# Optimization experiments

Measured on AMD Instinct MI355X. Metric: run time of the kernel, lower is better.

The kernel has to match this reference:

```python
import jax, jax.numpy as jnp
import numpy as np

N_NODES = 100000
N_EDGES = 3200000
IN_DIM = 768
HIDDEN = 128
CLASS_NUM = 2
N_GRAPHS = 512


def setup_inputs() -> dict:
    key = jax.random.key(0)
    ks = jax.random.split(key, 10)
    x = jax.random.normal(ks[0], (N_NODES, IN_DIM), dtype=jnp.float32)
    edge_index = jax.random.randint(ks[1], (2, N_EDGES), 0, N_NODES, dtype=jnp.int64)
    ptr = jnp.sort(jax.random.randint(ks[2], (N_GRAPHS + 1,), 0, N_NODES, dtype=jnp.int64))
    def glorot(k, shape):
        lim = jnp.sqrt(6.0 / (shape[0] + shape[1]))
        return jax.random.uniform(k, shape, jnp.float32, -lim, lim)
    W1 = glorot(ks[3], (IN_DIM, HIDDEN))
    b1 = jnp.zeros((HIDDEN,), jnp.float32)
    W2 = glorot(ks[4], (HIDDEN, HIDDEN))
    b2 = jnp.zeros((HIDDEN,), jnp.float32)
    Wc = glorot(ks[5], (HIDDEN, CLASS_NUM))
    bc = jnp.zeros((CLASS_NUM,), jnp.float32)
    return {"x": x, "edge_index": edge_index, "ptr": ptr,
            "W1": W1, "b1": b1, "W2": W2, "b2": b2, "Wc": Wc, "bc": bc}


def _gcn_conv(x, W, b, src, dst, norm, n_nodes):
    # PyG GCNConv: linear first, then normalized scatter-add aggregation, then bias
    h = x @ W                                  # [N, out]
    msg = h[src] * norm[:, None]               # gather + scale, [E+N, out]
    out = jax.ops.segment_sum(msg, dst, num_segments=n_nodes)
    return out + b


def reference(x, edge_index, ptr, W1, b1, W2, b2, Wc, bc):
    n = x.shape[0]
    loop = jnp.arange(n, dtype=edge_index.dtype)
    src = jnp.concatenate([edge_index[0], loop])  # add self-loops
    dst = jnp.concatenate([edge_index[1], loop])
    deg = jax.ops.segment_sum(jnp.ones_like(dst, dtype=x.dtype), dst, num_segments=n)
    dinv = jnp.where(deg > 0, jax.lax.rsqrt(deg), 0.0)
    norm = dinv[src] * dinv[dst]               # symmetric normalization
    h = jax.nn.relu(_gcn_conv(x, W1, b1, src, dst, norm, n))
    h = jax.nn.relu(_gcn_conv(h, W2, b2, src, dst, norm, n))
    out = _gcn_conv(h, Wc, bc, src, dst, norm, n)
    return out[ptr[:-1]]                       # first_pool: first node of each graph
```

## Files before the change

### kernel.cpp

```cpp
#include <hip/hip_runtime.h>

typedef short bf16x8 __attribute__((ext_vector_type(8)));
typedef float f32x4 __attribute__((ext_vector_type(4)));
typedef _Float16 f16x4 __attribute__((ext_vector_type(4)));

__device__ __forceinline__ unsigned short f2bf_rn(float x) {
    unsigned int u = __float_as_uint(x);
    unsigned int r = u + 0x7FFF + ((u >> 16) & 1);
    return (unsigned short)(r >> 16);
}
__device__ __forceinline__ float bf2f(unsigned short h) {
    return __uint_as_float(((unsigned int)h) << 16);
}


__global__ __launch_bounds__(256) void bucket_hist(const int* __restrict__ ei,
                                                   int* __restrict__ bcnt, int E, int NB) {
    __shared__ int h[1024];
    for (int i = threadIdx.x; i < NB; i += 256) h[i] = 0;
    __syncthreads();
    for (int e = blockIdx.x * blockDim.x + threadIdx.x; e < E; e += gridDim.x * blockDim.x) {
        atomicAdd(&h[ei[E + e] >> 7], 1);
    }
    __syncthreads();
    for (int i = threadIdx.x; i < NB; i += 256) {
        int v = h[i];
        if (v) atomicAdd(&bcnt[i], v);
    }
}

__global__ __launch_bounds__(1024) void bucket_scan(const int* __restrict__ bcnt,
                                                    int* __restrict__ bbase,
                                                    int* __restrict__ bcur,
                                                    int* __restrict__ offs,
                                                    int NB, int NN, int E) {
    __shared__ int s[1024];
    int t = threadIdx.x;
    int v = (t < NB) ? bcnt[t] : 0;
    s[t] = v;
    __syncthreads();
    for (int off = 1; off < 1024; off <<= 1) {
        int u = (t >= off) ? s[t - off] : 0;
        __syncthreads();
        s[t] += u;
        __syncthreads();
    }
    if (t < NB) {
        int base = s[t] - v;
        bbase[t] = base;
        bcur[t] = base;
    }
    if (t == 0) {
        bbase[NB] = E;
        offs[NN] = E;
    }
}

__global__ __launch_bounds__(256) void bucket_scatter(const int* __restrict__ ei,
                                                      int* __restrict__ bcur,
                                                      unsigned int* __restrict__ epk,
                                                      int E, int NB) {
    __shared__ int hist[1024];
    __shared__ int cur[1024];
    int tid = threadIdx.x;
    int chunk = (E + gridDim.x - 1) / gridDim.x;
    int beg = blockIdx.x * chunk;
    int end = beg + chunk; if (end > E) end = E;
    for (int i = tid; i < NB; i += 256) hist[i] = 0;
    __syncthreads();
    for (int e = beg + tid; e < end; e += 256) {
        atomicAdd(&hist[ei[E + e] >> 7], 1);
    }
    __syncthreads();
    for (int i = tid; i < NB; i += 256) {
        int c = hist[i];
        cur[i] = c ? atomicAdd(&bcur[i], c) : 0;
    }
    __syncthreads();
    for (int e = beg + tid; e < end; e += 256) {
        int s = ei[e];
        int d = ei[E + e];
        int p = atomicAdd(&cur[d >> 7], 1);
        epk[p] = ((unsigned)(d & 127) << 17) | (unsigned)s;
    }
}

__global__ __launch_bounds__(256) void bucket_build(const unsigned int* __restrict__ epk,
                                                    const int* __restrict__ bbase,
                                                    int* __restrict__ offs,
                                                    float* __restrict__ dinv,
                                                    int* __restrict__ srt,
                                                    int NN) {
    __shared__ int lcnt[128];
    __shared__ int sc[128];
    __shared__ int lcur[128];
    int b = blockIdx.x;
    int tid = threadIdx.x;
    int base = bbase[b], endp = bbase[b + 1];
    int ne = endp - base;
    int v0 = b << 7;
    int nv = NN - v0; if (nv > 128) nv = 128;

    if (tid < 128) lcnt[tid] = 0;
    __syncthreads();
    for (int i = tid; i < ne; i += 256) {
        int d = (int)(epk[base + i] >> 17);
        atomicAdd(&lcnt[d], 1);
    }
    __syncthreads();
    if (tid < 128) sc[tid] = lcnt[tid];
    __syncthreads();
    for (int off = 1; off < 128; off <<= 1) {
        int u = (tid < 128 && tid >= off) ? sc[tid - off] : 0;
        __syncthreads();
        if (tid < 128) sc[tid] += u;
        __syncthreads();
    }
    if (tid < nv) {
        int ex = sc[tid] - lcnt[tid];
        offs[v0 + tid] = base + ex;
        lcur[tid] = base + ex;
        dinv[v0 + tid] = rsqrtf((float)(lcnt[tid] + 1));
    }
    __syncthreads();
    for (int i = tid; i < ne; i += 256) {
        unsigned int pk = epk[base + i];
        int d = (int)(pk >> 17);
        int s = (int)(pk & 0x1FFFFu);
        int p = atomicAdd(&lcur[d], 1);
        srt[p] = s;
    }
}

__global__ void wt_prep(const float* __restrict__ W, unsigned short* __restrict__ hi,
                        unsigned short* __restrict__ lo, int K) {
    int idx = blockIdx.x * 256 + threadIdx.x;
    if (idx >= K * 128) return;
    int k = idx >> 7;
    int c = idx & 127;
    float x = W[idx];
    unsigned short h = f2bf_rn(x);
    unsigned short l = f2bf_rn(x - bf2f(h));
    hi[(size_t)c * K + k] = h;
    lo[(size_t)c * K + k] = l;
}

template <int K>
__global__ __launch_bounds__(256) void gemm_mfma(const float* __restrict__ X,
                                                 const unsigned short* __restrict__ Wt_hi,
                                                 const unsigned short* __restrict__ Wt_lo,
                                                 const float* __restrict__ dinv,
                                                 _Float16* __restrict__ G, int n) {
    __shared__ unsigned short As_hi[128][40];
    __shared__ unsigned short As_lo[128][40];
    __shared__ unsigned short Bs_hi[128][40];
    __shared__ unsigned short Bs_lo[128][40];

    const int tid = threadIdx.x;
    const int wave = tid >> 6;
    const int lane = tid & 63;
    const int l15 = lane & 15;
    const int l4 = lane >> 4;
    const int row0 = blockIdx.x * 128;
    const int wr0 = wave * 32;
    const size_t plane = (size_t)n * 16;

    f32x4 acc[2][8];
#pragma unroll
    for (int i = 0; i < 2; ++i)
#pragma unroll
        for (int j = 0; j < 8; ++j) acc[i][j] = (f32x4){0.f, 0.f, 0.f, 0.f};

    const int sr = tid >> 1;
    const int sf = (tid & 1) * 16;

    for (int k0 = 0; k0 < K; k0 += 32) {
        __syncthreads();
        {
            int grow = row0 + sr;
            float4 v[4];
            if (grow < n) {
                const float* src = X + (size_t)grow * K + k0 + sf;
#pragma unroll
                for (int g = 0; g < 4; ++g) v[g] = *(const float4*)(src + g * 4);
            } else {
#pragma unroll
                for (int g = 0; g < 4; ++g) v[g] = make_float4(0.f, 0.f, 0.f, 0.f);
            }
#pragma unroll
            for (int g = 0; g < 4; ++g) {
                ushort4 h, l;
                h.x = f2bf_rn(v[g].x); l.x = f2bf_rn(v[g].x - bf2f(h.x));
                h.y = f2bf_rn(v[g].y); l.y = f2bf_rn(v[g].y - bf2f(h.y));
                h.z = f2bf_rn(v[g].z); l.z = f2bf_rn(v[g].z - bf2f(h.z));
                h.w = f2bf_rn(v[g].w); l.w = f2bf_rn(v[g].w - bf2f(h.w));
                *(ushort4*)&As_hi[sr][sf + g * 4] = h;
                *(ushort4*)&As_lo[sr][sf + g * 4] = l;
            }
        }
        {
#pragma unroll
            for (int rep = 0; rep < 2; ++rep) {
                int id = tid + rep * 256;
                int c = id >> 2;
                int q = (id & 3) * 8;
                *(uint4*)&Bs_hi[c][q] = *(const uint4*)&Wt_hi[(size_t)c * K + k0 + q];
                *(uint4*)&Bs_lo[c][q] = *(const uint4*)&Wt_lo[(size_t)c * K + k0 + q];
            }
        }
        __syncthreads();
        bf16x8 ah[2], al[2];
#pragma unroll
        for (int i = 0; i < 2; ++i) {
            ah[i] = *(const bf16x8*)&As_hi[wr0 + i * 16 + l15][l4 * 8];
            al[i] = *(const bf16x8*)&As_lo[wr0 + i * 16 + l15][l4 * 8];
        }
#pragma unroll
        for (int j = 0; j < 8; ++j) {
            bf16x8 bh = *(const bf16x8*)&Bs_hi[j * 16 + l15][l4 * 8];
            bf16x8 bl = *(const bf16x8*)&Bs_lo[j * 16 + l15][l4 * 8];
#pragma unroll
            for (int i = 0; i < 2; ++i) {
                acc[i][j] = __builtin_amdgcn_mfma_f32_16x16x32_bf16(ah[i], bh, acc[i][j], 0, 0, 0);
                acc[i][j] = __builtin_amdgcn_mfma_f32_16x16x32_bf16(ah[i], bl, acc[i][j], 0, 0, 0);
                acc[i][j] = __builtin_amdgcn_mfma_f32_16x16x32_bf16(al[i], bh, acc[i][j], 0, 0, 0);
            }
        }
    }
#pragma unroll
    for (int i = 0; i < 2; ++i) {
#pragma unroll
        for (int r = 0; r < 4; ++r) {
            int grow = row0 + wr0 + i * 16 + l4 * 4 + r;
            if (grow < n) {
                float dv = dinv[grow];
#pragma unroll
                for (int j = 0; j < 8; ++j) {
                    G[plane * j + (size_t)grow * 16 + l15] = (_Float16)(acc[i][j][r] * dv);
                }
            }
        }
    }
}

__global__ __launch_bounds__(256) void aggregate_slice4(const _Float16* __restrict__ G,
                                                        const int* __restrict__ offs,
                                                        const int* __restrict__ srt,
                                                        const float* __restrict__ dinv,
                                                        const float* __restrict__ bias,
                                                        float* __restrict__ H, int n, int do_relu) {
    int bid = blockIdx.x;
    int slice = bid & 7;
    int wave = threadIdx.x >> 6;
    int lane = threadIdx.x & 63;
    int sub = lane >> 4;
    int slot = (lane >> 2) & 3;
    int q = lane & 3;
    int node = (bid >> 3) * 16 + wave * 4 + sub;
    if (node >= n) return;
    const _Float16* __restrict__ Gp = G + (size_t)slice * (size_t)n * 16;
    int beg = offs[node], end = offs[node + 1];
    float a0 = 0.f, a1 = 0.f, a2 = 0.f, a3 = 0.f;
    int e = beg + slot;
    for (; e + 4 < end; e += 8) {
        int s0 = srt[e], s1 = srt[e + 4];
        f16x4 v0 = *(const f16x4*)(Gp + (size_t)s0 * 16 + q * 4);
        f16x4 v1 = *(const f16x4*)(Gp + (size_t)s1 * 16 + q * 4);
        a0 += (float)v0[0] + (float)v1[0];
        a1 += (float)v0[1] + (float)v1[1];
        a2 += (float)v0[2] + (float)v1[2];
        a3 += (float)v0[3] + (float)v1[3];
    }
    if (e < end) {
        int s = srt[e];
        f16x4 v = *(const f16x4*)(Gp + (size_t)s * 16 + q * 4);
        a0 += (float)v[0]; a1 += (float)v[1]; a2 += (float)v[2]; a3 += (float)v[3];
    }
    a0 += __shfl_xor(a0, 4);  a1 += __shfl_xor(a1, 4);  a2 += __shfl_xor(a2, 4);  a3 += __shfl_xor(a3, 4);
    a0 += __shfl_xor(a0, 8);  a1 += __shfl_xor(a1, 8);  a2 += __shfl_xor(a2, 8);  a3 += __shfl_xor(a3, 8);
    if (slot == 0) {
        f16x4 sv = *(const f16x4*)(Gp + (size_t)node * 16 + q * 4);
        a0 += (float)sv[0]; a1 += (float)sv[1]; a2 += (float)sv[2]; a3 += (float)sv[3];
        float dv = dinv[node];
        float4 b = *(const float4*)&bias[slice * 16 + q * 4];
        float4 r;
        r.x = a0 * dv + b.x;
        r.y = a1 * dv + b.y;
        r.z = a2 * dv + b.z;
        r.w = a3 * dv + b.w;
        if (do_relu) {
            r.x = fmaxf(r.x, 0.f); r.y = fmaxf(r.y, 0.f);
            r.z = fmaxf(r.z, 0.f); r.w = fmaxf(r.w, 0.f);
        }
        *(float4*)&H[(size_t)node * 128 + slice * 16 + q * 4] = r;
    }
}

__global__ __launch_bounds__(256) void gemm_c2_kernel(const float* __restrict__ H,
                                                      const float* __restrict__ Wc,
                                                      const float* __restrict__ dinv,
                                                      float* __restrict__ G3, int n) {
    int wid = (blockIdx.x * blockDim.x + threadIdx.x) >> 6;
    int lane = threadIdx.x & 63;
    if (wid >= n) return;
    float2 h = *(const float2*)&H[(size_t)wid * 128 + lane * 2];
    float w00 = Wc[lane * 4 + 0];
    float w01 = Wc[lane * 4 + 1];
    float w10 = Wc[lane * 4 + 2];
    float w11 = Wc[lane * 4 + 3];
    float p0 = h.x * w00 + h.y * w10;
    float p1 = h.x * w01 + h.y * w11;
    for (int off = 32; off > 0; off >>= 1) {
        p0 += __shfl_xor(p0, off);
        p1 += __shfl_xor(p1, off);
    }
    if (lane == 0) {
        float dv = dinv[wid];
        G3[(size_t)wid * 2 + 0] = p0 * dv;
        G3[(size_t)wid * 2 + 1] = p1 * dv;
    }
}

__global__ __launch_bounds__(64) void final_kernel(const float* __restrict__ G3,
                                                   const int* __restrict__ ptr,
                                                   const int* __restrict__ offs,
                                                   const int* __restrict__ srt,
                                                   const float* __restrict__ dinv,
                                                   const float* __restrict__ bc,
                                                   float* __restrict__ out, int ngraphs) {
    int i = blockIdx.x;
    if (i >= ngraphs) return;
    int v = ptr[i];
    int lane = threadIdx.x;
    float p0 = 0.f, p1 = 0.f;
    int beg = offs[v], end = offs[v + 1];
    for (int e = beg + lane; e < end; e += 64) {
        int s = srt[e];
        p0 += G3[(size_t)s * 2 + 0];
        p1 += G3[(size_t)s * 2 + 1];
    }
    for (int off = 32; off > 0; off >>= 1) {
        p0 += __shfl_xor(p0, off);
        p1 += __shfl_xor(p1, off);
    }
    if (lane == 0) {
        p0 += G3[(size_t)v * 2 + 0];
        p1 += G3[(size_t)v * 2 + 1];
        float dv = dinv[v];
        out[i * 2 + 0] = p0 * dv + bc[0];
        out[i * 2 + 1] = p1 * dv + bc[1];
    }
}

extern "C" void kernel_launch(void* const* d_in, const int* in_sizes, int n_in,
                              void* d_out, int out_size, void* d_ws, size_t ws_size,
                              hipStream_t stream) {
    const float* x  = (const float*)d_in[0];
    const int* ei   = (const int*)d_in[1];
    const int* ptr  = (const int*)d_in[2];
    const float* W1 = (const float*)d_in[3];
    const float* b1 = (const float*)d_in[4];
    const float* W2 = (const float*)d_in[5];
    const float* b2 = (const float*)d_in[6];
    const float* Wc = (const float*)d_in[7];
    const float* bc = (const float*)d_in[8];
    float* out = (float*)d_out;

    const int IN_DIM = 768, HID = 128;
    const int NN = in_sizes[0] / IN_DIM;
    const int E  = in_sizes[1] / 2;
    const int NG = in_sizes[2] - 1;
    const int NB = (NN + 127) >> 7;

    char* ws = (char*)d_ws;
    size_t off = 0;
    auto alloc = [&](size_t bytes) -> void* {
        void* p = ws + off;
        off += (bytes + 255) & ~(size_t)255;
        return p;
    };
    float* dinv   = (float*)alloc((size_t)NN * 4);
    int*   offs   = (int*)alloc((size_t)(NN + 1) * 4);
    int*   bcnt   = (int*)alloc((size_t)(NB + 1) * 4);
    int*   bbase  = (int*)alloc((size_t)(NB + 1) * 4);
    int*   bcur   = (int*)alloc((size_t)NB * 4);
    int*   srt    = (int*)alloc((size_t)E * 4);
    _Float16* G   = (_Float16*)alloc((size_t)NN * HID * 2);
    float* H      = (float*)alloc((size_t)NN * HID * 4);
    float* G3     = (float*)alloc((size_t)NN * 2 * 4);
    unsigned short* Wt1_hi = (unsigned short*)alloc((size_t)IN_DIM * HID * 2);
    unsigned short* Wt1_lo = (unsigned short*)alloc((size_t)IN_DIM * HID * 2);
    unsigned short* Wt2_hi = (unsigned short*)alloc((size_t)HID * HID * 2);
    unsigned short* Wt2_lo = (unsigned short*)alloc((size_t)HID * HID * 2);

    unsigned int* epk = (unsigned int*)H;

    (void)n_in; (void)out_size; (void)ws_size;

    hipMemsetAsync(bcnt, 0, (size_t)(NB + 1) * 4, stream);
    bucket_hist<<<512, 256, 0, stream>>>(ei, bcnt, E, NB);
    bucket_scan<<<1, 1024, 0, stream>>>(bcnt, bbase, bcur, offs, NB, NN, E);
    bucket_scatter<<<256, 256, 0, stream>>>(ei, bcur, epk, E, NB);
    bucket_build<<<NB, 256, 0, stream>>>(epk, bbase, offs, dinv, srt, NN);

    wt_prep<<<(IN_DIM * HID + 255) / 256, 256, 0, stream>>>(W1, Wt1_hi, Wt1_lo, IN_DIM);
    wt_prep<<<(HID * HID + 255) / 256, 256, 0, stream>>>(W2, Wt2_hi, Wt2_lo, HID);

    int gblocks = (NN + 127) / 128;
    int slice_blocks = ((NN + 15) / 16) * 8;
    int wpn_blocks = (NN * 64 + 255) / 256;

    gemm_mfma<768><<<gblocks, 256, 0, stream>>>(x, Wt1_hi, Wt1_lo, dinv, G, NN);
    aggregate_slice4<<<slice_blocks, 256, 0, stream>>>(G, offs, srt, dinv, b1, H, NN, 1);
    gemm_mfma<128><<<gblocks, 256, 0, stream>>>(H, Wt2_hi, Wt2_lo, dinv, G, NN);
    aggregate_slice4<<<slice_blocks, 256, 0, stream>>>(G, offs, srt, dinv, b2, H, NN, 1);
    gemm_c2_kernel<<<wpn_blocks, 256, 0, stream>>>(H, Wc, dinv, G3, NN);
    final_kernel<<<NG, 64, 0, stream>>>(G3, ptr, offs, srt, dinv, bc, out, NG);
}
```

Baseline: 603.9 us.

## Widen aggregation slices to 32 features and store prescaled byte offsets

The GEMM output layout changes from eight 16-feature planes to four 32-feature planes. Each gathered neighbor row is now 64 contiguous bytes instead of 32, and the aggregation kernel reads it with 8 lanes per row. The sorted source indices are stored pre-shifted by 6 so the gather computes the address without a multiply, and the final kernel shifts them back. The inner gather loop is also unrolled to four edges per iteration. This halves the number of passes over the index array, lengthens each random access segment, and adds more loads in flight, at the cost of more registers and a slightly different reduction layout.

```diff
diff --git a/kernel.cpp b/kernel.cpp
--- a/kernel.cpp
+++ b/kernel.cpp
@@ -128,7 +128,7 @@
         int d = (int)(pk >> 17);
         int s = (int)(pk & 0x1FFFFu);
         int p = atomicAdd(&lcur[d], 1);
-        srt[p] = s;
+        srt[p] = s << 6;
     }
 }
 
@@ -163,7 +163,7 @@
     const int l4 = lane >> 4;
     const int row0 = blockIdx.x * 128;
     const int wr0 = wave * 32;
-    const size_t plane = (size_t)n * 16;
+    const size_t plane = (size_t)n * 32;
 
     f32x4 acc[2][8];
 #pragma unroll
@@ -236,53 +236,55 @@
                 float dv = dinv[grow];
 #pragma unroll
                 for (int j = 0; j < 8; ++j) {
-                    G[plane * j + (size_t)grow * 16 + l15] = (_Float16)(acc[i][j][r] * dv);
+                    G[plane * (j >> 1) + (size_t)grow * 32 + (j & 1) * 16 + l15] =
+                        (_Float16)(acc[i][j][r] * dv);
                 }
             }
         }
     }
 }
 
-__global__ __launch_bounds__(256) void aggregate_slice4(const _Float16* __restrict__ G,
-                                                        const int* __restrict__ offs,
-                                                        const int* __restrict__ srt,
-                                                        const float* __restrict__ dinv,
-                                                        const float* __restrict__ bias,
-                                                        float* __restrict__ H, int n, int do_relu) {
+__global__ __launch_bounds__(256) void aggregate_slice32(const _Float16* __restrict__ G,
+                                                         const int* __restrict__ offs,
+                                                         const int* __restrict__ srt,
+                                                         const float* __restrict__ dinv,
+                                                         const float* __restrict__ bias,
+                                                         float* __restrict__ H, int n, int do_relu) {
     int bid = blockIdx.x;
-    int slice = bid & 7;
+    int slice = bid & 3;
     int wave = threadIdx.x >> 6;
     int lane = threadIdx.x & 63;
-    int sub = lane >> 4;
-    int slot = (lane >> 2) & 3;
-    int q = lane & 3;
-    int node = (bid >> 3) * 16 + wave * 4 + sub;
+    int sub = lane >> 5;
+    int slot = (lane >> 3) & 3;
+    int q = lane & 7;
+    int node = (bid >> 2) * 8 + wave * 2 + sub;
     if (node >= n) return;
-    const _Float16* __restrict__ Gp = G + (size_t)slice * (size_t)n * 16;
+    const char* __restrict__ Gb = (const char*)G + (size_t)slice * (size_t)n * 64 + q * 8;
     int beg = offs[node], end = offs[node + 1];
     float a0 = 0.f, a1 = 0.f, a2 = 0.f, a3 = 0.f;
     int e = beg + slot;
-    for (; e + 4 < end; e += 8) {
-        int s0 = srt[e], s1 = srt[e + 4];
-        f16x4 v0 = *(const f16x4*)(Gp + (size_t)s0 * 16 + q * 4);
-        f16x4 v1 = *(const f16x4*)(Gp + (size_t)s1 * 16 + q * 4);
-        a0 += (float)v0[0] + (float)v1[0];
-        a1 += (float)v0[1] + (float)v1[1];
-        a2 += (float)v0[2] + (float)v1[2];
-        a3 += (float)v0[3] + (float)v1[3];
-    }
-    if (e < end) {
-        int s = srt[e];
-        f16x4 v = *(const f16x4*)(Gp + (size_t)s * 16 + q * 4);
+    for (; e + 12 < end; e += 16) {
+        int o0 = srt[e], o1 = srt[e + 4], o2 = srt[e + 8], o3 = srt[e + 12];
+        f16x4 v0 = *(const f16x4*)(Gb + o0);
+        f16x4 v1 = *(const f16x4*)(Gb + o1);
+        f16x4 v2 = *(const f16x4*)(Gb + o2);
+        f16x4 v3 = *(const f16x4*)(Gb + o3);
+        a0 += (float)v0[0] + (float)v1[0] + (float)v2[0] + (float)v3[0];
+        a1 += (float)v0[1] + (float)v1[1] + (float)v2[1] + (float)v3[1];
+        a2 += (float)v0[2] + (float)v1[2] + (float)v2[2] + (float)v3[2];
+        a3 += (float)v0[3] + (float)v1[3] + (float)v2[3] + (float)v3[3];
+    }
+    for (; e < end; e += 4) {
+        f16x4 v = *(const f16x4*)(Gb + srt[e]);
         a0 += (float)v[0]; a1 += (float)v[1]; a2 += (float)v[2]; a3 += (float)v[3];
     }
-    a0 += __shfl_xor(a0, 4);  a1 += __shfl_xor(a1, 4);  a2 += __shfl_xor(a2, 4);  a3 += __shfl_xor(a3, 4);
     a0 += __shfl_xor(a0, 8);  a1 += __shfl_xor(a1, 8);  a2 += __shfl_xor(a2, 8);  a3 += __shfl_xor(a3, 8);
+    a0 += __shfl_xor(a0, 16); a1 += __shfl_xor(a1, 16); a2 += __shfl_xor(a2, 16); a3 += __shfl_xor(a3, 16);
     if (slot == 0) {
-        f16x4 sv = *(const f16x4*)(Gp + (size_t)node * 16 + q * 4);
+        f16x4 sv = *(const f16x4*)(Gb + ((size_t)node << 6));
         a0 += (float)sv[0]; a1 += (float)sv[1]; a2 += (float)sv[2]; a3 += (float)sv[3];
         float dv = dinv[node];
-        float4 b = *(const float4*)&bias[slice * 16 + q * 4];
+        float4 b = *(const float4*)&bias[slice * 32 + q * 4];
         float4 r;
         r.x = a0 * dv + b.x;
         r.y = a1 * dv + b.y;
@@ -292,7 +294,7 @@
             r.x = fmaxf(r.x, 0.f); r.y = fmaxf(r.y, 0.f);
             r.z = fmaxf(r.z, 0.f); r.w = fmaxf(r.w, 0.f);
         }
-        *(float4*)&H[(size_t)node * 128 + slice * 16 + q * 4] = r;
+        *(float4*)&H[(size_t)node * 128 + slice * 32 + q * 4] = r;
     }
 }
 
@@ -335,7 +337,7 @@
     float p0 = 0.f, p1 = 0.f;
     int beg = offs[v], end = offs[v + 1];
     for (int e = beg + lane; e < end; e += 64) {
-        int s = srt[e];
+        int s = srt[e] >> 6;
         p0 += G3[(size_t)s * 2 + 0];
         p1 += G3[(size_t)s * 2 + 1];
     }
@@ -407,13 +409,13 @@
     wt_prep<<<(HID * HID + 255) / 256, 256, 0, stream>>>(W2, Wt2_hi, Wt2_lo, HID);
 
     int gblocks = (NN + 127) / 128;
-    int slice_blocks = ((NN + 15) / 16) * 8;
+    int slice_blocks = ((NN + 7) / 8) * 4;
     int wpn_blocks = (NN * 64 + 255) / 256;
 
     gemm_mfma<768><<<gblocks, 256, 0, stream>>>(x, Wt1_hi, Wt1_lo, dinv, G, NN);
-    aggregate_slice4<<<slice_blocks, 256, 0, stream>>>(G, offs, srt, dinv, b1, H, NN, 1);
+    aggregate_slice32<<<slice_blocks, 256, 0, stream>>>(G, offs, srt, dinv, b1, H, NN, 1);
     gemm_mfma<128><<<gblocks, 256, 0, stream>>>(H, Wt2_hi, Wt2_lo, dinv, G, NN);
-    aggregate_slice4<<<slice_blocks, 256, 0, stream>>>(G, offs, srt, dinv, b2, H, NN, 1);
+    aggregate_slice32<<<slice_blocks, 256, 0, stream>>>(G, offs, srt, dinv, b2, H, NN, 1);
     gemm_c2_kernel<<<wpn_blocks, 256, 0, stream>>>(H, Wc, dinv, G3, NN);
     final_kernel<<<NG, 64, 0, stream>>>(G3, ptr, offs, srt, dinv, bc, out, NG);
 }
```

New measurement: 572.6 us. 1.05x faster.
